# Kernel optimization log

Hardware: AMD Instinct MI355X
Metric: run time of the kernel (lower is better)

Reference implementation:

```python
import jax, jax.numpy as jnp
import numpy as np

B, S, H, A = 2, 512, 256, 128


def setup_inputs() -> dict:
    key = jax.random.key(0)
    k1, k2, k3, k4 = jax.random.split(key, 4)
    x = jax.random.normal(k1, (B, S, H), dtype=jnp.float32)
    attention_mask = jax.random.randint(k2, (B, S), 0, 2, dtype=jnp.int32)
    # xavier_normal for w_a, standard normal for query (as in torch init)
    w_a = jax.random.normal(k3, (H, A), dtype=jnp.float32) * np.sqrt(2.0 / (H + A))
    query = jax.random.normal(k4, (A,), dtype=jnp.float32)
    return {"x": x, "attention_mask": attention_mask, "w_a": w_a, "query": query}


def reference(x, attention_mask, w_a, query):
    # attention_type == 'fixed' path of SelfAttention
    b, s, h = x.shape
    tri = jnp.tril(jnp.ones((s, s), dtype=x.dtype))  # tri[i,j]=1 iff j<=i (causal)
    # values[b,i,j,h] = x[b,j,h] if j<=i else 0  (the O(S^2*H) masked broadcast)
    values = tri[None, :, :, None] * x[:, None, :, :]          # (B,S,S,H)
    key_t = jnp.tanh(jnp.einsum('bijh,ha->bija', values, w_a))  # (B,S,S,A)
    temp = jnp.einsum('a,bija->bij', query, key_t)              # (B,S,S)
    # additive softmax mask: 0 on lower triangle, -inf above diagonal
    smask = jnp.where(tri == 1, 0.0, -jnp.inf).astype(x.dtype)
    d = jax.nn.softmax(temp + smask, axis=-1)                   # (B,S,S)
    am = (attention_mask[:, :s] != 0)
    pair = (am[:, :, None] & am[:, None, :]).astype(d.dtype)    # (B,S,S)
    d = d * pair
    a = jnp.einsum('bij,bjh->bih', d, x)                        # (B,S,H)
    return (a, d)
```

## Files before the change

kernel.cpp:

```cpp
#include <hip/hip_runtime.h>
#include <math.h>

#define BB 2
#define SS 512
#define HH 256
#define AA 128
#define CH 4
#define NCH (SS / CH)

__global__ void k_tc(const float* __restrict__ x,
                     const int* __restrict__ am,
                     const float* __restrict__ w_a,
                     const float* __restrict__ query,
                     float* __restrict__ Ews,
                     float* __restrict__ Cws) {
    const int blk  = blockIdx.x;
    const int b    = blk >> 7;
    const int c    = blk & 127;
    const int j0   = c * CH;
    const int tid  = threadIdx.x;
    const int a    = tid & 127;
    const int half = tid >> 7;

    __shared__ float xs[CH][HH];
    __shared__ float sred[CH][2][AA];
    __shared__ float Wl[CH];

    const float4* xr4 = (const float4*)(x + (size_t)(b * SS + j0) * HH);
    ((float4*)&xs[0][0])[tid] = xr4[tid];
    __syncthreads();

    float acc0 = 0.f, acc1 = 0.f, acc2 = 0.f, acc3 = 0.f;
    const int hbase = half * 128;
    for (int hh = 0; hh < 128; hh += 4) {
        const int h = hbase + hh;
        const float w0 = w_a[(h + 0) * AA + a];
        const float w1 = w_a[(h + 1) * AA + a];
        const float w2 = w_a[(h + 2) * AA + a];
        const float w3 = w_a[(h + 3) * AA + a];
        const float4 x0 = *(const float4*)&xs[0][h];
        const float4 x1 = *(const float4*)&xs[1][h];
        const float4 x2 = *(const float4*)&xs[2][h];
        const float4 x3 = *(const float4*)&xs[3][h];
        acc0 = fmaf(x0.x, w0, fmaf(x0.y, w1, fmaf(x0.z, w2, fmaf(x0.w, w3, acc0))));
        acc1 = fmaf(x1.x, w0, fmaf(x1.y, w1, fmaf(x1.z, w2, fmaf(x1.w, w3, acc1))));
        acc2 = fmaf(x2.x, w0, fmaf(x2.y, w1, fmaf(x2.z, w2, fmaf(x2.w, w3, acc2))));
        acc3 = fmaf(x3.x, w0, fmaf(x3.y, w1, fmaf(x3.z, w2, fmaf(x3.w, w3, acc3))));
    }
    sred[0][half][a] = acc0;
    sred[1][half][a] = acc1;
    sred[2][half][a] = acc2;
    sred[3][half][a] = acc3;
    __syncthreads();

    const int wvi  = tid >> 6;
    const int lane = tid & 63;
    {
        const int r = wvi;
        const float f0 = sred[r][0][lane]      + sred[r][1][lane];
        const float f1 = sred[r][0][lane + 64] + sred[r][1][lane + 64];
        float v = tanhf(f0) * query[lane] + tanhf(f1) * query[lane + 64];
        for (int off = 32; off > 0; off >>= 1)
            v += __shfl_down(v, off, 64);
        if (lane == 0) {
            const float e = expf(v);
            Wl[r] = am[b * SS + j0 + r] ? e : 0.f;
            Ews[b * SS + j0 + r] = e;
        }
    }
    __syncthreads();

    const float cacc = fmaf(Wl[0], xs[0][tid],
                       fmaf(Wl[1], xs[1][tid],
                       fmaf(Wl[2], xs[2][tid],
                            Wl[3] * xs[3][tid])));
    Cws[(size_t)(b * NCH + c) * HH + tid] = cacc;
}

__global__ void k_out(const float* __restrict__ Ews,
                      const float* __restrict__ Cws,
                      const int* __restrict__ am,
                      const float* __restrict__ x,
                      float* __restrict__ dout,
                      float* __restrict__ aout) {
    const int blk  = blockIdx.x;
    const int b    = blk >> 7;
    const int i0   = (blk & 127) << 2;
    const int tid  = threadIdx.x;
    const int lane = tid & 63;
    const int wvi  = tid >> 6;

    __shared__ float Es[SS];
    __shared__ float Ws[SS];
    __shared__ float red[4];
    __shared__ float Pinv[4];

    const float e0 = Ews[b * SS + tid];
    const float e1 = Ews[b * SS + tid + 256];
    const int  am0 = am[b * SS + tid];
    const int  am1 = am[b * SS + tid + 256];
    Es[tid] = e0;             Es[tid + 256] = e1;
    Ws[tid] = am0 ? e0 : 0.f; Ws[tid + 256] = am1 ? e1 : 0.f;

    float p = ((tid <= i0) ? e0 : 0.f) + ((tid + 256 <= i0) ? e1 : 0.f);
    for (int off = 32; off > 0; off >>= 1)
        p += __shfl_down(p, off, 64);
    if (lane == 0) red[wvi] = p;
    __syncthreads();
    if (tid == 0) {
        const float P0 = red[0] + red[1] + red[2] + red[3];
        const float P1 = P0 + Es[i0 + 1];
        const float P2 = P1 + Es[i0 + 2];
        const float P3 = P2 + Es[i0 + 3];
        Pinv[0] = 1.f / P0; Pinv[1] = 1.f / P1;
        Pinv[2] = 1.f / P2; Pinv[3] = 1.f / P3;
    }
    __syncthreads();

    const int* amg = am + b * SS;
    int ami[4];
#pragma unroll
    for (int r = 0; r < 4; ++r) ami[r] = amg[i0 + r];

    const size_t drow = (size_t)(b * SS + i0) * SS;
    const int c4  = tid & 127;
    const int jc  = c4 << 2;
    const float4 wv4 = *(const float4*)&Ws[jc];
#pragma unroll
    for (int pp = 0; pp < 2; ++pp) {
        const int   r  = (tid >> 7) + 2 * pp;
        const int   i  = i0 + r;
        const float pv = Pinv[r];
        const bool  on = ami[r] != 0;
        float4 o;
        o.x = (on && jc + 0 <= i) ? wv4.x * pv : 0.f;
        o.y = (on && jc + 1 <= i) ? wv4.y * pv : 0.f;
        o.z = (on && jc + 2 <= i) ? wv4.z * pv : 0.f;
        o.w = (on && jc + 3 <= i) ? wv4.w * pv : 0.f;
        *(float4*)&dout[drow + (size_t)r * SS + jc] = o;
    }

    const int nfull = i0 >> 2;
    const float* xb = x + (size_t)b * SS * HH + tid;
    const float* Cb = Cws + (size_t)b * NCH * HH + tid;

    float s0 = 0.f, s1 = 0.f, s2 = 0.f, s3 = 0.f;
    int cc = 0;
    for (; cc + 4 <= nfull; cc += 4) {
        s0 += Cb[(size_t)(cc + 0) * HH];
        s1 += Cb[(size_t)(cc + 1) * HH];
        s2 += Cb[(size_t)(cc + 2) * HH];
        s3 += Cb[(size_t)(cc + 3) * HH];
    }
    for (; cc < nfull; ++cc)
        s0 += Cb[(size_t)cc * HH];
    const float base = (s0 + s1) + (s2 + s3);

    const float a0v = fmaf(Ws[i0],     xb[(size_t)(i0)     * HH], base);
    const float a1v = fmaf(Ws[i0 + 1], xb[(size_t)(i0 + 1) * HH], a0v);
    const float a2v = fmaf(Ws[i0 + 2], xb[(size_t)(i0 + 2) * HH], a1v);
    const float a3v = fmaf(Ws[i0 + 3], xb[(size_t)(i0 + 3) * HH], a2v);

    const size_t arow = (size_t)(b * SS + i0) * HH + tid;
    const float av[4] = {a0v, a1v, a2v, a3v};
#pragma unroll
    for (int r = 0; r < 4; ++r)
        aout[arow + (size_t)r * HH] = ami[r] ? av[r] * Pinv[r] : 0.f;
}

extern "C" void kernel_launch(void* const* d_in, const int* in_sizes, int n_in,
                              void* d_out, int out_size, void* d_ws, size_t ws_size,
                              hipStream_t stream) {
    const float* x     = (const float*)d_in[0];
    const int*   am    = (const int*)d_in[1];
    const float* w_a   = (const float*)d_in[2];
    const float* query = (const float*)d_in[3];

    float* a_out  = (float*)d_out;
    float* d_outp = a_out + (size_t)BB * SS * HH;

    float* Ews = (float*)d_ws;
    float* Cws = Ews + BB * SS;

    k_tc <<<BB * NCH,    256, 0, stream>>>(x, am, w_a, query, Ews, Cws);
    k_out<<<BB * SS / 4, 256, 0, stream>>>(Ews, Cws, am, x, d_outp, a_out);
}
```

Baseline: 76.06 us.

## Fuse score and output kernels with a software grid barrier

Merges the two kernels into one 256-block, 512-thread launch. A global atomic-counter grid barrier separates the score phase from the softmax/output phase, which removes one launch and reuses the x rows already held in shared memory. The projection now uses float4 weight loads split across 16 h-slices with a shared-memory reduction, the prefix sum over chunks is split across two thread groups, and outputs use nontemporal stores. The grid barrier assumes all 256 blocks are co-resident and could deadlock if they are not; it relies on the launch bounds allowing 2 blocks per CU.

```diff
diff --git a/kernel.cpp b/kernel.cpp
--- a/kernel.cpp
+++ b/kernel.cpp
@@ -7,165 +7,188 @@
 #define AA 128
 #define CH 4
 #define NCH (SS / CH)
-
-__global__ void k_tc(const float* __restrict__ x,
-                     const int* __restrict__ am,
-                     const float* __restrict__ w_a,
-                     const float* __restrict__ query,
-                     float* __restrict__ Ews,
-                     float* __restrict__ Cws) {
-    const int blk  = blockIdx.x;
-    const int b    = blk >> 7;
-    const int c    = blk & 127;
-    const int j0   = c * CH;
-    const int tid  = threadIdx.x;
-    const int a    = tid & 127;
-    const int half = tid >> 7;
+#define NBLK (BB * NCH)
+#define NT 512
+
+typedef float f4_t __attribute__((ext_vector_type(4)));
+
+__device__ unsigned g_tick = 0;
+
+__global__ __launch_bounds__(NT, 2)
+void k_fused(const float* __restrict__ x,
+             const int* __restrict__ am,
+             const float* __restrict__ w_a,
+             const float* __restrict__ query,
+             float* __restrict__ Ews,
+             float* __restrict__ Cws,
+             float* __restrict__ dout,
+             float* __restrict__ aout) {
+    const int blk = blockIdx.x;
+    const int b   = blk >> 7;
+    const int c   = blk & 127;
+    const int j0  = c * CH;
+    const int tid = threadIdx.x;
 
     __shared__ float xs[CH][HH];
-    __shared__ float sred[CH][2][AA];
+    __shared__ float pred[16][CH][AA];
+    __shared__ float redr[CH][2];
     __shared__ float Wl[CH];
-
-    const float4* xr4 = (const float4*)(x + (size_t)(b * SS + j0) * HH);
-    ((float4*)&xs[0][0])[tid] = xr4[tid];
-    __syncthreads();
-
-    float acc0 = 0.f, acc1 = 0.f, acc2 = 0.f, acc3 = 0.f;
-    const int hbase = half * 128;
-    for (int hh = 0; hh < 128; hh += 4) {
-        const int h = hbase + hh;
-        const float w0 = w_a[(h + 0) * AA + a];
-        const float w1 = w_a[(h + 1) * AA + a];
-        const float w2 = w_a[(h + 2) * AA + a];
-        const float w3 = w_a[(h + 3) * AA + a];
-        const float4 x0 = *(const float4*)&xs[0][h];
-        const float4 x1 = *(const float4*)&xs[1][h];
-        const float4 x2 = *(const float4*)&xs[2][h];
-        const float4 x3 = *(const float4*)&xs[3][h];
-        acc0 = fmaf(x0.x, w0, fmaf(x0.y, w1, fmaf(x0.z, w2, fmaf(x0.w, w3, acc0))));
-        acc1 = fmaf(x1.x, w0, fmaf(x1.y, w1, fmaf(x1.z, w2, fmaf(x1.w, w3, acc1))));
-        acc2 = fmaf(x2.x, w0, fmaf(x2.y, w1, fmaf(x2.z, w2, fmaf(x2.w, w3, acc2))));
-        acc3 = fmaf(x3.x, w0, fmaf(x3.y, w1, fmaf(x3.z, w2, fmaf(x3.w, w3, acc3))));
-    }
-    sred[0][half][a] = acc0;
-    sred[1][half][a] = acc1;
-    sred[2][half][a] = acc2;
-    sred[3][half][a] = acc3;
-    __syncthreads();
-
-    const int wvi  = tid >> 6;
-    const int lane = tid & 63;
-    {
-        const int r = wvi;
-        const float f0 = sred[r][0][lane]      + sred[r][1][lane];
-        const float f1 = sred[r][0][lane + 64] + sred[r][1][lane + 64];
-        float v = tanhf(f0) * query[lane] + tanhf(f1) * query[lane + 64];
-        for (int off = 32; off > 0; off >>= 1)
-            v += __shfl_down(v, off, 64);
-        if (lane == 0) {
-            const float e = expf(v);
-            Wl[r] = am[b * SS + j0 + r] ? e : 0.f;
-            Ews[b * SS + j0 + r] = e;
-        }
-    }
-    __syncthreads();
-
-    const float cacc = fmaf(Wl[0], xs[0][tid],
-                       fmaf(Wl[1], xs[1][tid],
-                       fmaf(Wl[2], xs[2][tid],
-                            Wl[3] * xs[3][tid])));
-    Cws[(size_t)(b * NCH + c) * HH + tid] = cacc;
-}
-
-__global__ void k_out(const float* __restrict__ Ews,
-                      const float* __restrict__ Cws,
-                      const int* __restrict__ am,
-                      const float* __restrict__ x,
-                      float* __restrict__ dout,
-                      float* __restrict__ aout) {
-    const int blk  = blockIdx.x;
-    const int b    = blk >> 7;
-    const int i0   = (blk & 127) << 2;
-    const int tid  = threadIdx.x;
-    const int lane = tid & 63;
-    const int wvi  = tid >> 6;
-
     __shared__ float Es[SS];
     __shared__ float Ws[SS];
-    __shared__ float red[4];
-    __shared__ float Pinv[4];
-
-    const float e0 = Ews[b * SS + tid];
-    const float e1 = Ews[b * SS + tid + 256];
-    const int  am0 = am[b * SS + tid];
-    const int  am1 = am[b * SS + tid + 256];
-    Es[tid] = e0;             Es[tid + 256] = e1;
-    Ws[tid] = am0 ? e0 : 0.f; Ws[tid + 256] = am1 ? e1 : 0.f;
-
-    float p = ((tid <= i0) ? e0 : 0.f) + ((tid + 256 <= i0) ? e1 : 0.f);
-    for (int off = 32; off > 0; off >>= 1)
-        p += __shfl_down(p, off, 64);
-    if (lane == 0) red[wvi] = p;
-    __syncthreads();
+    __shared__ float cpar[2][HH];
+    __shared__ float Pinv[CH];
+    __shared__ float red8[8];
+    __shared__ int   amis[CH];
+
+    {
+        const float2* src = (const float2*)(x + (size_t)(b * SS + j0) * HH);
+        ((float2*)&xs[0][0])[tid] = src[tid];
+    }
+    __syncthreads();
+
+    const int q  = tid & 31;
+    const int hs = tid >> 5;
+    const int h0 = hs << 4;
+    float4 acc0 = make_float4(0.f, 0.f, 0.f, 0.f);
+    float4 acc1 = acc0, acc2 = acc0, acc3 = acc0;
+    const float4* w4 = (const float4*)w_a;
+
+#define ROWFMA(ACC, R)                                                          \
+    {                                                                           \
+        const float4 xv = *(const float4*)&xs[R][h];                            \
+        ACC.x = fmaf(xv.x, wa.x, fmaf(xv.y, wb.x, fmaf(xv.z, wc.x, fmaf(xv.w, wd.x, ACC.x)))); \
+        ACC.y = fmaf(xv.x, wa.y, fmaf(xv.y, wb.y, fmaf(xv.z, wc.y, fmaf(xv.w, wd.y, ACC.y)))); \
+        ACC.z = fmaf(xv.x, wa.z, fmaf(xv.y, wb.z, fmaf(xv.z, wc.z, fmaf(xv.w, wd.z, ACC.z)))); \
+        ACC.w = fmaf(xv.x, wa.w, fmaf(xv.y, wb.w, fmaf(xv.z, wc.w, fmaf(xv.w, wd.w, ACC.w)))); \
+    }
+
+#pragma unroll
+    for (int hh = 0; hh < 16; hh += 4) {
+        const int h = h0 + hh;
+        const float4 wa = w4[(h + 0) * (AA / 4) + q];
+        const float4 wb = w4[(h + 1) * (AA / 4) + q];
+        const float4 wc = w4[(h + 2) * (AA / 4) + q];
+        const float4 wd = w4[(h + 3) * (AA / 4) + q];
+        ROWFMA(acc0, 0)
+        ROWFMA(acc1, 1)
+        ROWFMA(acc2, 2)
+        ROWFMA(acc3, 3)
+    }
+#undef ROWFMA
+
+    *(float4*)&pred[hs][0][q << 2] = acc0;
+    *(float4*)&pred[hs][1][q << 2] = acc1;
+    *(float4*)&pred[hs][2][q << 2] = acc2;
+    *(float4*)&pred[hs][3][q << 2] = acc3;
+    __syncthreads();
+
+    {
+        const int r = tid >> 7;
+        const int a = tid & 127;
+        float s = 0.f;
+#pragma unroll
+        for (int t = 0; t < 16; ++t) s += pred[t][r][a];
+        float v = tanhf(s) * query[a];
+#pragma unroll
+        for (int off = 32; off; off >>= 1) v += __shfl_down(v, off, 64);
+        if ((tid & 63) == 0) redr[r][(tid >> 6) & 1] = v;
+    }
+    if (tid < CH) amis[tid] = am[b * SS + j0 + tid];
+    __syncthreads();
+    if (tid < CH) {
+        const float t = redr[tid][0] + redr[tid][1];
+        const float e = expf(t);
+        Wl[tid] = amis[tid] ? e : 0.f;
+        Ews[b * SS + j0 + tid] = e;
+    }
+    __syncthreads();
+
+    if (tid < HH) {
+        const float cacc = fmaf(Wl[0], xs[0][tid],
+                           fmaf(Wl[1], xs[1][tid],
+                           fmaf(Wl[2], xs[2][tid],
+                                Wl[3] * xs[3][tid])));
+        Cws[(size_t)(b * NCH + c) * HH + tid] = cacc;
+    }
+    __syncthreads();
+
     if (tid == 0) {
-        const float P0 = red[0] + red[1] + red[2] + red[3];
-        const float P1 = P0 + Es[i0 + 1];
-        const float P2 = P1 + Es[i0 + 2];
-        const float P3 = P2 + Es[i0 + 3];
+        const unsigned old =
+            __hip_atomic_fetch_add(&g_tick, 1u, __ATOMIC_RELEASE, __HIP_MEMORY_SCOPE_AGENT);
+        const unsigned target = (old / NBLK + 1u) * NBLK;
+        while (__hip_atomic_load(&g_tick, __ATOMIC_RELAXED, __HIP_MEMORY_SCOPE_AGENT) < target)
+            __builtin_amdgcn_s_sleep(2);
+        (void)__hip_atomic_load(&g_tick, __ATOMIC_ACQUIRE, __HIP_MEMORY_SCOPE_AGENT);
+    }
+    __syncthreads();
+
+    {
+        const float e = Ews[b * SS + tid];
+        const int  m  = am[b * SS + tid];
+        Es[tid] = e;
+        Ws[tid] = m ? e : 0.f;
+        float p = (tid <= j0) ? e : 0.f;
+#pragma unroll
+        for (int off = 32; off; off >>= 1) p += __shfl_down(p, off, 64);
+        if ((tid & 63) == 0) red8[tid >> 6] = p;
+    }
+    __syncthreads();
+    if (tid == 0) {
+        const float P0 = ((red8[0] + red8[1]) + (red8[2] + red8[3]))
+                       + ((red8[4] + red8[5]) + (red8[6] + red8[7]));
+        const float P1 = P0 + Es[j0 + 1];
+        const float P2 = P1 + Es[j0 + 2];
+        const float P3 = P2 + Es[j0 + 3];
         Pinv[0] = 1.f / P0; Pinv[1] = 1.f / P1;
         Pinv[2] = 1.f / P2; Pinv[3] = 1.f / P3;
     }
     __syncthreads();
 
-    const int* amg = am + b * SS;
-    int ami[4];
-#pragma unroll
-    for (int r = 0; r < 4; ++r) ami[r] = amg[i0 + r];
-
-    const size_t drow = (size_t)(b * SS + i0) * SS;
-    const int c4  = tid & 127;
-    const int jc  = c4 << 2;
-    const float4 wv4 = *(const float4*)&Ws[jc];
-#pragma unroll
-    for (int pp = 0; pp < 2; ++pp) {
-        const int   r  = (tid >> 7) + 2 * pp;
-        const int   i  = i0 + r;
+    {
+        const int   r  = tid >> 7;
+        const int   jc = (tid & 127) << 2;
+        const int   i  = j0 + r;
         const float pv = Pinv[r];
-        const bool  on = ami[r] != 0;
-        float4 o;
-        o.x = (on && jc + 0 <= i) ? wv4.x * pv : 0.f;
-        o.y = (on && jc + 1 <= i) ? wv4.y * pv : 0.f;
-        o.z = (on && jc + 2 <= i) ? wv4.z * pv : 0.f;
-        o.w = (on && jc + 3 <= i) ? wv4.w * pv : 0.f;
-        *(float4*)&dout[drow + (size_t)r * SS + jc] = o;
-    }
-
-    const int nfull = i0 >> 2;
-    const float* xb = x + (size_t)b * SS * HH + tid;
-    const float* Cb = Cws + (size_t)b * NCH * HH + tid;
-
-    float s0 = 0.f, s1 = 0.f, s2 = 0.f, s3 = 0.f;
-    int cc = 0;
-    for (; cc + 4 <= nfull; cc += 4) {
-        s0 += Cb[(size_t)(cc + 0) * HH];
-        s1 += Cb[(size_t)(cc + 1) * HH];
-        s2 += Cb[(size_t)(cc + 2) * HH];
-        s3 += Cb[(size_t)(cc + 3) * HH];
-    }
-    for (; cc < nfull; ++cc)
-        s0 += Cb[(size_t)cc * HH];
-    const float base = (s0 + s1) + (s2 + s3);
-
-    const float a0v = fmaf(Ws[i0],     xb[(size_t)(i0)     * HH], base);
-    const float a1v = fmaf(Ws[i0 + 1], xb[(size_t)(i0 + 1) * HH], a0v);
-    const float a2v = fmaf(Ws[i0 + 2], xb[(size_t)(i0 + 2) * HH], a1v);
-    const float a3v = fmaf(Ws[i0 + 3], xb[(size_t)(i0 + 3) * HH], a2v);
-
-    const size_t arow = (size_t)(b * SS + i0) * HH + tid;
-    const float av[4] = {a0v, a1v, a2v, a3v};
-#pragma unroll
-    for (int r = 0; r < 4; ++r)
-        aout[arow + (size_t)r * HH] = ami[r] ? av[r] * Pinv[r] : 0.f;
+        const bool  on = amis[r] != 0;
+        const float4 wv = *(const float4*)&Ws[jc];
+        f4_t o;
+        o.x = (on && jc + 0 <= i) ? wv.x * pv : 0.f;
+        o.y = (on && jc + 1 <= i) ? wv.y * pv : 0.f;
+        o.z = (on && jc + 2 <= i) ? wv.z * pv : 0.f;
+        o.w = (on && jc + 3 <= i) ? wv.w * pv : 0.f;
+        __builtin_nontemporal_store(o, (f4_t*)&dout[(size_t)(b * SS + i) * SS + jc]);
+    }
+
+    {
+        const int g = tid >> 8;
+        const int h = tid & 255;
+        const int nfull = c;
+        const float* Cb = Cws + (size_t)b * NCH * HH + h;
+        float s0 = 0.f, s1 = 0.f, s2 = 0.f, s3 = 0.f;
+        int cc = g;
+        for (; cc + 7 <= nfull; cc += 8) {
+            s0 += Cb[(size_t)(cc + 0) * HH];
+            s1 += Cb[(size_t)(cc + 2) * HH];
+            s2 += Cb[(size_t)(cc + 4) * HH];
+            s3 += Cb[(size_t)(cc + 6) * HH];
+        }
+        for (; cc < nfull; cc += 2) s0 += Cb[(size_t)cc * HH];
+        cpar[g][h] = (s0 + s1) + (s2 + s3);
+    }
+    __syncthreads();
+    if (tid < HH) {
+        const int   h    = tid;
+        const float base = cpar[0][h] + cpar[1][h];
+        const float a0 = fmaf(Ws[j0 + 0], xs[0][h], base);
+        const float a1 = fmaf(Ws[j0 + 1], xs[1][h], a0);
+        const float a2 = fmaf(Ws[j0 + 2], xs[2][h], a1);
+        const float a3 = fmaf(Ws[j0 + 3], xs[3][h], a2);
+        const size_t arow = (size_t)(b * SS + j0) * HH + h;
+        __builtin_nontemporal_store(amis[0] ? a0 * Pinv[0] : 0.f, &aout[arow + 0 * HH]);
+        __builtin_nontemporal_store(amis[1] ? a1 * Pinv[1] : 0.f, &aout[arow + 1 * HH]);
+        __builtin_nontemporal_store(amis[2] ? a2 * Pinv[2] : 0.f, &aout[arow + 2 * HH]);
+        __builtin_nontemporal_store(amis[3] ? a3 * Pinv[3] : 0.f, &aout[arow + 3 * HH]);
+    }
 }
 
 extern "C" void kernel_launch(void* const* d_in, const int* in_sizes, int n_in,
@@ -182,6 +205,5 @@
     float* Ews = (float*)d_ws;
     float* Cws = Ews + BB * SS;
 
-    k_tc <<<BB * NCH,    256, 0, stream>>>(x, am, w_a, query, Ews, Cws);
-    k_out<<<BB * SS / 4, 256, 0, stream>>>(Ews, Cws, am, x, d_outp, a_out);
+    k_fused<<<NBLK, NT, 0, stream>>>(x, am, w_a, query, Ews, Cws, d_outp, a_out);
 }
```

Measured after the change: 77.41 us. No clear change (+1.8%).
